# Kernel optimization log

Measured on AMD Instinct MI355X. Metric: run time of the kernel, lower is better.

Reference implementation:

```python
import jax, jax.numpy as jnp
import numpy as np

STEP = 3
INTERVAL = STEP // 2          # 1
W_LEN = 2 * INTERVAL + 1      # sliding window length = 3
N_TOK = 2 * STEP + 1          # tokens per position (reg + window + diff) = 7


def setup_inputs() -> dict:
    key = jax.random.key(0)
    k1, k2, k3, k4 = jax.random.split(key, 4)
    b, n, d, r = 8, 1024, 1024, 256
    x = jax.random.normal(k1, (b, n, d), dtype=jnp.float32)
    mask = jnp.ones((b, N_TOK, 1), dtype=jnp.float32)
    # nn.Linear(input_dim, red_dim, bias=False) weight: (red_dim, input_dim)
    W = jax.random.normal(k2, (r, d), dtype=jnp.float32) / np.sqrt(d).astype(np.float32)
    pos_local = jax.random.normal(k3, (1, N_TOK, r), dtype=jnp.float32)
    reg_token = jax.random.normal(k4, (1, 1, r), dtype=jnp.float32)
    pad_tokens = jnp.zeros((1, INTERVAL, d), dtype=jnp.float32)
    return {"x": x, "mask": mask, "W": W, "pos_local": pos_local,
            "reg_token": reg_token, "pad_tokens": pad_tokens}


def reference(x, mask, W, pos_local, reg_token, pad_tokens):
    # Faithful, vectorized version of the 'local' branch (dropout in eval mode).
    b, n, d = x.shape
    r = W.shape[0]
    pad = jnp.broadcast_to(pad_tokens, (b, INTERVAL, d))
    xp = jnp.concatenate([pad, x, pad], axis=1)            # (b, n + 2*INTERVAL, d)
    # torch loop runs i in [INTERVAL, n): m computed positions; first INTERVAL rows of x_ stay zero
    m = n - INTERVAL
    idx = jnp.arange(m)[:, None] + jnp.arange(W_LEN)[None, :]   # (m, W_LEN), window starts at i-INTERVAL
    wins = xp[:, idx]                                        # (b, m, W_LEN, d)
    center = wins[:, :, INTERVAL][:, :, None, :]             # (b, m, 1, d)
    x_new = jnp.concatenate([wins, wins - center], axis=2)   # (b, m, 2*W_LEN, d)
    y = jnp.einsum('bmwd,rd->bmwr', x_new, W)                # reduce_embedding, no bias
    reg = jnp.broadcast_to(reg_token.reshape(1, 1, 1, r), (b, m, 1, r))
    out = (jnp.concatenate([reg, y], axis=2) + pos_local[None]) * mask[:, None]  # (b, m, N_TOK, r)
    # first INTERVAL sequence positions were never written (remain zero)
    out = jnp.concatenate([jnp.zeros((b, INTERVAL, N_TOK, r), out.dtype), out], axis=1)
    return out
```

## Files before the change

kernel.cpp:

```cpp
#include <hip/hip_runtime.h>

#define BB 8
#define NN 1024
#define DD 1024
#define RR 256
#define MM (BB * NN)
#define NTOK 7

typedef __bf16 bf16x8 __attribute__((ext_vector_type(8)));
typedef float f32x4 __attribute__((ext_vector_type(4)));

__global__ __launch_bounds__(256) void wcvt(const float* __restrict__ W, __bf16* __restrict__ Wb) {
  const int i = (blockIdx.x * 256 + threadIdx.x) * 4;
  float4 v = *reinterpret_cast<const float4*>(W + i);
  union { __bf16 b[4]; ushort4 u; } p;
  p.b[0] = (__bf16)v.x; p.b[1] = (__bf16)v.y; p.b[2] = (__bf16)v.z; p.b[3] = (__bf16)v.w;
  *reinterpret_cast<ushort4*>(Wb + i) = p.u;
}

__device__ __forceinline__ bf16x8 cvt8(const float4& lo, const float4& hi) {
  bf16x8 r;
  r[0] = (__bf16)lo.x; r[1] = (__bf16)lo.y; r[2] = (__bf16)lo.z; r[3] = (__bf16)lo.w;
  r[4] = (__bf16)hi.x; r[5] = (__bf16)hi.y; r[6] = (__bf16)hi.z; r[7] = (__bf16)hi.w;
  return r;
}

__global__ __launch_bounds__(256) void gemm_mfma(const float* __restrict__ X,
                                                 const __bf16* __restrict__ Wb,
                                                 float* __restrict__ P) {
  const int tid = threadIdx.x;
  const int wave = tid >> 6;
  const int lane = tid & 63;
  const int m0 = blockIdx.x * 32;
  const int c0 = wave * 64;
  const int lr = lane & 15;
  const int lg = lane >> 4;

  const float*  xb0 = X  + (size_t)(m0 + lr) * DD + lg * 8;
  const float*  xb1 = xb0 + (size_t)16 * DD;
  const __bf16* wb  = Wb + (size_t)(c0 + lr) * DD + lg * 8;

  f32x4 acc[2][4] = {};

  float4 a0[2][2], a1[2][2];
  bf16x8 b0[4], b1[4];

#define LD_A(dst, kk) do {                                          \
    dst[0][0] = *reinterpret_cast<const float4*>(xb0 + (kk));       \
    dst[0][1] = *reinterpret_cast<const float4*>(xb0 + (kk) + 4);   \
    dst[1][0] = *reinterpret_cast<const float4*>(xb1 + (kk));       \
    dst[1][1] = *reinterpret_cast<const float4*>(xb1 + (kk) + 4);   \
  } while (0)
#define LD_B(dst, kk) do {                                          \
    dst[0] = *reinterpret_cast<const bf16x8*>(wb + (kk));           \
    dst[1] = *reinterpret_cast<const bf16x8*>(wb + 16 * DD + (kk)); \
    dst[2] = *reinterpret_cast<const bf16x8*>(wb + 32 * DD + (kk)); \
    dst[3] = *reinterpret_cast<const bf16x8*>(wb + 48 * DD + (kk)); \
  } while (0)
#define MFMA_STEP(aS, bS) do {                                      \
    bf16x8 af0 = cvt8(aS[0][0], aS[0][1]);                          \
    bf16x8 af1 = cvt8(aS[1][0], aS[1][1]);                          \
    acc[0][0] = __builtin_amdgcn_mfma_f32_16x16x32_bf16(af0, bS[0], acc[0][0], 0, 0, 0); \
    acc[1][0] = __builtin_amdgcn_mfma_f32_16x16x32_bf16(af1, bS[0], acc[1][0], 0, 0, 0); \
    acc[0][1] = __builtin_amdgcn_mfma_f32_16x16x32_bf16(af0, bS[1], acc[0][1], 0, 0, 0); \
    acc[1][1] = __builtin_amdgcn_mfma_f32_16x16x32_bf16(af1, bS[1], acc[1][1], 0, 0, 0); \
    acc[0][2] = __builtin_amdgcn_mfma_f32_16x16x32_bf16(af0, bS[2], acc[0][2], 0, 0, 0); \
    acc[1][2] = __builtin_amdgcn_mfma_f32_16x16x32_bf16(af1, bS[2], acc[1][2], 0, 0, 0); \
    acc[0][3] = __builtin_amdgcn_mfma_f32_16x16x32_bf16(af0, bS[3], acc[0][3], 0, 0, 0); \
    acc[1][3] = __builtin_amdgcn_mfma_f32_16x16x32_bf16(af1, bS[3], acc[1][3], 0, 0, 0); \
  } while (0)

  LD_A(a0, 0); LD_B(b0, 0);
  for (int k0 = 0; k0 < DD - 64; k0 += 64) {
    LD_A(a1, k0 + 32); LD_B(b1, k0 + 32);
    MFMA_STEP(a0, b0);
    LD_A(a0, k0 + 64); LD_B(b0, k0 + 64);
    MFMA_STEP(a1, b1);
  }
  LD_A(a1, DD - 32); LD_B(b1, DD - 32);
  MFMA_STEP(a0, b0);
  MFMA_STEP(a1, b1);

#undef LD_A
#undef LD_B
#undef MFMA_STEP

#pragma unroll
  for (int mi = 0; mi < 2; ++mi)
#pragma unroll
    for (int ni = 0; ni < 4; ++ni) {
      const int col = c0 + ni * 16 + lr;
#pragma unroll
      for (int r = 0; r < 4; ++r) {
        const int row = m0 + mi * 16 + lg * 4 + r;
        P[(size_t)row * RR + col] = acc[mi][ni][r];
      }
    }
}

__global__ void pad_proj(const float* __restrict__ Wt, const float* __restrict__ pad,
                         float* __restrict__ Ppad) {
  const int c = blockIdx.x;
  const int lane = threadIdx.x;
  float s = 0.f;
  for (int k = lane; k < DD; k += 64) s += Wt[(size_t)c * DD + k] * pad[k];
#pragma unroll
  for (int off = 32; off; off >>= 1) s += __shfl_down(s, off);
  if (lane == 0) Ppad[c] = s;
}

__global__ __launch_bounds__(256) void assemble(const float* __restrict__ P,
                                                const float* __restrict__ Ppad,
                                                const float* __restrict__ mask,
                                                const float* __restrict__ pos,
                                                const float* __restrict__ regtok,
                                                float* __restrict__ out) {
  const size_t gid = (size_t)blockIdx.x * blockDim.x + threadIdx.x;
  const int c = (int)(gid & 63) * 4;
  const int j = (int)((gid >> 6) & (NN - 1));
  const int b = (int)(gid >> 16);

  float* outp = out + (((size_t)b * NN + j) * NTOK) * RR + c;

  if (j == 0) {
    float4 z = make_float4(0.f, 0.f, 0.f, 0.f);
#pragma unroll
    for (int t = 0; t < NTOK; ++t)
      *reinterpret_cast<float4*>(outp + (size_t)t * RR) = z;
    return;
  }

  const int i = j - 1;
  float4 q[3];
#pragma unroll
  for (int w = 0; w < 3; ++w) {
    const int src = i + w - 1;
    q[w] = (src < 0)
               ? *reinterpret_cast<const float4*>(Ppad + c)
               : *reinterpret_cast<const float4*>(P + ((size_t)b * NN + src) * RR + c);
  }
  const float4 rg = *reinterpret_cast<const float4*>(regtok + c);

  float mk[NTOK];
#pragma unroll
  for (int t = 0; t < NTOK; ++t) mk[t] = mask[b * NTOK + t];

#pragma unroll
  for (int t = 0; t < NTOK; ++t) {
    const float4 ps = *reinterpret_cast<const float4*>(pos + (size_t)t * RR + c);
    float4 v;
    if (t == 0) {
      v = rg;
    } else if (t <= 3) {
      v = q[t - 1];
    } else {
      const int w = t - 4;
      v = make_float4(q[w].x - q[1].x, q[w].y - q[1].y, q[w].z - q[1].z, q[w].w - q[1].w);
    }
    v.x = (v.x + ps.x) * mk[t];
    v.y = (v.y + ps.y) * mk[t];
    v.z = (v.z + ps.z) * mk[t];
    v.w = (v.w + ps.w) * mk[t];
    *reinterpret_cast<float4*>(outp + (size_t)t * RR) = v;
  }
}

extern "C" void kernel_launch(void* const* d_in, const int* in_sizes, int n_in,
                              void* d_out, int out_size, void* d_ws, size_t ws_size,
                              hipStream_t stream) {
  const float* x      = (const float*)d_in[0];
  const float* mask   = (const float*)d_in[1];
  const float* W      = (const float*)d_in[2];
  const float* pos    = (const float*)d_in[3];
  const float* regtok = (const float*)d_in[4];
  const float* pad    = (const float*)d_in[5];
  float* out = (float*)d_out;

  float*   P    = (float*)d_ws;
  __bf16*  Wb   = (__bf16*)((char*)d_ws + (size_t)MM * RR * 4);
  float*   Ppad = (float*)((char*)d_ws + (size_t)MM * RR * 4 + (size_t)RR * DD * 2);

  wcvt<<<RR * DD / (256 * 4), 256, 0, stream>>>(W, Wb);
  gemm_mfma<<<MM / 32, 256, 0, stream>>>(x, Wb, P);
  pad_proj<<<RR, 64, 0, stream>>>(W, pad, Ppad);
  assemble<<<(BB * NN * 64) / 256, 256, 0, stream>>>(P, Ppad, mask, pos, regtok, out);
}
```

Measured before the change: 138.4 us.

## Fuse output assembly into GEMM epilogue with halo rows and cleanup kernel

The GEMM now produces 16-row tiles, stages them in shared memory, and directly writes the 7-token output for the interior positions of each tile, so the full projection matrix no longer has to round-trip through global memory. Only the two boundary rows at each tile edge go to a halo buffer, and a small cleanup kernel fills in the output positions whose windows cross tile edges. Halving the M tile cuts per-block reuse of the W operand, which doubles W reads, and adds LDS use and an extra launch.

```diff
diff --git a/kernel.cpp b/kernel.cpp
--- a/kernel.cpp
+++ b/kernel.cpp
@@ -18,6 +18,17 @@
   *reinterpret_cast<ushort4*>(Wb + i) = p.u;
 }
 
+__global__ void pad_proj(const float* __restrict__ Wt, const float* __restrict__ pad,
+                         float* __restrict__ Ppad) {
+  const int c = blockIdx.x;
+  const int lane = threadIdx.x;
+  float s = 0.f;
+  for (int k = lane; k < DD; k += 64) s += Wt[(size_t)c * DD + k] * pad[k];
+#pragma unroll
+  for (int off = 32; off; off >>= 1) s += __shfl_down(s, off);
+  if (lane == 0) Ppad[c] = s;
+}
+
 __device__ __forceinline__ bf16x8 cvt8(const float4& lo, const float4& hi) {
   bf16x8 r;
   r[0] = (__bf16)lo.x; r[1] = (__bf16)lo.y; r[2] = (__bf16)lo.z; r[3] = (__bf16)lo.w;
@@ -25,31 +36,32 @@
   return r;
 }
 
-__global__ __launch_bounds__(256) void gemm_mfma(const float* __restrict__ X,
-                                                 const __bf16* __restrict__ Wb,
-                                                 float* __restrict__ P) {
+__global__ __launch_bounds__(256) void gemm_fused(const float* __restrict__ X,
+                                                  const __bf16* __restrict__ Wb,
+                                                  const float* __restrict__ Ppad,
+                                                  const float* __restrict__ mask,
+                                                  const float* __restrict__ pos,
+                                                  const float* __restrict__ regtok,
+                                                  float* __restrict__ Phalo,
+                                                  float* __restrict__ out) {
   const int tid = threadIdx.x;
   const int wave = tid >> 6;
   const int lane = tid & 63;
-  const int m0 = blockIdx.x * 32;
+  const int m0 = blockIdx.x * 16;
   const int c0 = wave * 64;
   const int lr = lane & 15;
   const int lg = lane >> 4;
 
-  const float*  xb0 = X  + (size_t)(m0 + lr) * DD + lg * 8;
-  const float*  xb1 = xb0 + (size_t)16 * DD;
-  const __bf16* wb  = Wb + (size_t)(c0 + lr) * DD + lg * 8;
-
-  f32x4 acc[2][4] = {};
-
-  float4 a0[2][2], a1[2][2];
-  bf16x8 b0[4], b1[4];
+  const float*  xb = X  + (size_t)(m0 + lr) * DD + lg * 8;
+  const __bf16* wb = Wb + (size_t)(c0 + lr) * DD + lg * 8;
+
+  f32x4 acc[4] = {};
+  float4 aA[2], aB[2];
+  bf16x8 bA[4], bB[4];
 
 #define LD_A(dst, kk) do {                                          \
-    dst[0][0] = *reinterpret_cast<const float4*>(xb0 + (kk));       \
-    dst[0][1] = *reinterpret_cast<const float4*>(xb0 + (kk) + 4);   \
-    dst[1][0] = *reinterpret_cast<const float4*>(xb1 + (kk));       \
-    dst[1][1] = *reinterpret_cast<const float4*>(xb1 + (kk) + 4);   \
+    dst[0] = *reinterpret_cast<const float4*>(xb + (kk));           \
+    dst[1] = *reinterpret_cast<const float4*>(xb + (kk) + 4);       \
   } while (0)
 #define LD_B(dst, kk) do {                                          \
     dst[0] = *reinterpret_cast<const bf16x8*>(wb + (kk));           \
@@ -58,96 +70,120 @@
     dst[3] = *reinterpret_cast<const bf16x8*>(wb + 48 * DD + (kk)); \
   } while (0)
 #define MFMA_STEP(aS, bS) do {                                      \
-    bf16x8 af0 = cvt8(aS[0][0], aS[0][1]);                          \
-    bf16x8 af1 = cvt8(aS[1][0], aS[1][1]);                          \
-    acc[0][0] = __builtin_amdgcn_mfma_f32_16x16x32_bf16(af0, bS[0], acc[0][0], 0, 0, 0); \
-    acc[1][0] = __builtin_amdgcn_mfma_f32_16x16x32_bf16(af1, bS[0], acc[1][0], 0, 0, 0); \
-    acc[0][1] = __builtin_amdgcn_mfma_f32_16x16x32_bf16(af0, bS[1], acc[0][1], 0, 0, 0); \
-    acc[1][1] = __builtin_amdgcn_mfma_f32_16x16x32_bf16(af1, bS[1], acc[1][1], 0, 0, 0); \
-    acc[0][2] = __builtin_amdgcn_mfma_f32_16x16x32_bf16(af0, bS[2], acc[0][2], 0, 0, 0); \
-    acc[1][2] = __builtin_amdgcn_mfma_f32_16x16x32_bf16(af1, bS[2], acc[1][2], 0, 0, 0); \
-    acc[0][3] = __builtin_amdgcn_mfma_f32_16x16x32_bf16(af0, bS[3], acc[0][3], 0, 0, 0); \
-    acc[1][3] = __builtin_amdgcn_mfma_f32_16x16x32_bf16(af1, bS[3], acc[1][3], 0, 0, 0); \
+    bf16x8 af = cvt8(aS[0], aS[1]);                                 \
+    acc[0] = __builtin_amdgcn_mfma_f32_16x16x32_bf16(af, bS[0], acc[0], 0, 0, 0); \
+    acc[1] = __builtin_amdgcn_mfma_f32_16x16x32_bf16(af, bS[1], acc[1], 0, 0, 0); \
+    acc[2] = __builtin_amdgcn_mfma_f32_16x16x32_bf16(af, bS[2], acc[2], 0, 0, 0); \
+    acc[3] = __builtin_amdgcn_mfma_f32_16x16x32_bf16(af, bS[3], acc[3], 0, 0, 0); \
   } while (0)
 
-  LD_A(a0, 0); LD_B(b0, 0);
+  LD_A(aA, 0); LD_B(bA, 0);
   for (int k0 = 0; k0 < DD - 64; k0 += 64) {
-    LD_A(a1, k0 + 32); LD_B(b1, k0 + 32);
-    MFMA_STEP(a0, b0);
-    LD_A(a0, k0 + 64); LD_B(b0, k0 + 64);
-    MFMA_STEP(a1, b1);
-  }
-  LD_A(a1, DD - 32); LD_B(b1, DD - 32);
-  MFMA_STEP(a0, b0);
-  MFMA_STEP(a1, b1);
+    LD_A(aB, k0 + 32); LD_B(bB, k0 + 32);
+    MFMA_STEP(aA, bA);
+    LD_A(aA, k0 + 64); LD_B(bA, k0 + 64);
+    MFMA_STEP(aB, bB);
+  }
+  LD_A(aB, DD - 32); LD_B(bB, DD - 32);
+  MFMA_STEP(aA, bA);
+  MFMA_STEP(aB, bB);
 
 #undef LD_A
 #undef LD_B
 #undef MFMA_STEP
 
-#pragma unroll
-  for (int mi = 0; mi < 2; ++mi)
-#pragma unroll
-    for (int ni = 0; ni < 4; ++ni) {
-      const int col = c0 + ni * 16 + lr;
-#pragma unroll
-      for (int r = 0; r < 4; ++r) {
-        const int row = m0 + mi * 16 + lg * 4 + r;
-        P[(size_t)row * RR + col] = acc[mi][ni][r];
+  __shared__ float Pt[16][260];
+#pragma unroll
+  for (int ni = 0; ni < 4; ++ni)
+#pragma unroll
+    for (int r = 0; r < 4; ++r)
+      Pt[lg * 4 + r][c0 + ni * 16 + lr] = acc[ni][r];
+  __syncthreads();
+
+  const int c4 = (tid & 63) * 4;
+
+  {
+    const int hr = tid >> 6;
+    const int row = (hr < 2) ? hr : hr + 12;
+    float4 v = *reinterpret_cast<const float4*>(&Pt[row][c4]);
+    *reinterpret_cast<float4*>(&Phalo[(size_t)(m0 + row) * RR + c4]) = v;
+  }
+
+  const int b  = m0 >> 10;
+  const int n0 = m0 & (NN - 1);
+
+  float mk[NTOK];
+#pragma unroll
+  for (int t = 0; t < NTOK; ++t) mk[t] = mask[b * NTOK + t];
+  const float4 rg = *reinterpret_cast<const float4*>(regtok + c4);
+  float4 psv[NTOK];
+#pragma unroll
+  for (int t = 0; t < NTOK; ++t)
+    psv[t] = *reinterpret_cast<const float4*>(pos + (size_t)t * RR + c4);
+
+  const int jlo = (n0 == 0) ? 0 : n0 + 2;
+  for (int j = jlo + wave; j < n0 + 16; j += 4) {
+    float* outp = out + (((size_t)b * NN + j) * NTOK) * RR + c4;
+    if (j == 0) {
+      float4 z = make_float4(0.f, 0.f, 0.f, 0.f);
+#pragma unroll
+      for (int t = 0; t < NTOK; ++t)
+        *reinterpret_cast<float4*>(outp + (size_t)t * RR) = z;
+      continue;
+    }
+    float4 q[3];
+#pragma unroll
+    for (int w = 0; w < 3; ++w) {
+      const int src = j - 2 + w;
+      q[w] = (src < 0) ? *reinterpret_cast<const float4*>(Ppad + c4)
+                       : *reinterpret_cast<const float4*>(&Pt[src - n0][c4]);
+    }
+#pragma unroll
+    for (int t = 0; t < NTOK; ++t) {
+      float4 v;
+      if (t == 0) {
+        v = rg;
+      } else if (t <= 3) {
+        v = q[t - 1];
+      } else {
+        const int w = t - 4;
+        v = make_float4(q[w].x - q[1].x, q[w].y - q[1].y, q[w].z - q[1].z, q[w].w - q[1].w);
       }
-    }
-}
-
-__global__ void pad_proj(const float* __restrict__ Wt, const float* __restrict__ pad,
-                         float* __restrict__ Ppad) {
-  const int c = blockIdx.x;
-  const int lane = threadIdx.x;
-  float s = 0.f;
-  for (int k = lane; k < DD; k += 64) s += Wt[(size_t)c * DD + k] * pad[k];
-#pragma unroll
-  for (int off = 32; off; off >>= 1) s += __shfl_down(s, off);
-  if (lane == 0) Ppad[c] = s;
-}
-
-__global__ __launch_bounds__(256) void assemble(const float* __restrict__ P,
-                                                const float* __restrict__ Ppad,
-                                                const float* __restrict__ mask,
-                                                const float* __restrict__ pos,
-                                                const float* __restrict__ regtok,
-                                                float* __restrict__ out) {
-  const size_t gid = (size_t)blockIdx.x * blockDim.x + threadIdx.x;
-  const int c = (int)(gid & 63) * 4;
-  const int j = (int)((gid >> 6) & (NN - 1));
-  const int b = (int)(gid >> 16);
-
-  float* outp = out + (((size_t)b * NN + j) * NTOK) * RR + c;
-
-  if (j == 0) {
-    float4 z = make_float4(0.f, 0.f, 0.f, 0.f);
-#pragma unroll
-    for (int t = 0; t < NTOK; ++t)
-      *reinterpret_cast<float4*>(outp + (size_t)t * RR) = z;
-    return;
-  }
-
-  const int i = j - 1;
+      v.x = (v.x + psv[t].x) * mk[t];
+      v.y = (v.y + psv[t].y) * mk[t];
+      v.z = (v.z + psv[t].z) * mk[t];
+      v.w = (v.w + psv[t].w) * mk[t];
+      *reinterpret_cast<float4*>(outp + (size_t)t * RR) = v;
+    }
+  }
+}
+
+#define NCLEAN_ROWS (BB * 126)
+__global__ __launch_bounds__(256) void cleanup(const float* __restrict__ Phalo,
+                                               const float* __restrict__ mask,
+                                               const float* __restrict__ pos,
+                                               const float* __restrict__ regtok,
+                                               float* __restrict__ out) {
+  const int gid = blockIdx.x * 256 + threadIdx.x;
+  const int rowIdx = gid >> 6;
+  if (rowIdx >= NCLEAN_ROWS) return;
+  const int b  = rowIdx / 126;
+  const int rr = rowIdx - b * 126;
+  const int j  = 16 * ((rr >> 1) + 1) + (rr & 1);
+  const int c4 = (gid & 63) * 4;
+
   float4 q[3];
 #pragma unroll
-  for (int w = 0; w < 3; ++w) {
-    const int src = i + w - 1;
-    q[w] = (src < 0)
-               ? *reinterpret_cast<const float4*>(Ppad + c)
-               : *reinterpret_cast<const float4*>(P + ((size_t)b * NN + src) * RR + c);
-  }
-  const float4 rg = *reinterpret_cast<const float4*>(regtok + c);
-
-  float mk[NTOK];
-#pragma unroll
-  for (int t = 0; t < NTOK; ++t) mk[t] = mask[b * NTOK + t];
+  for (int w = 0; w < 3; ++w)
+    q[w] = *reinterpret_cast<const float4*>(&Phalo[((size_t)b * NN + j - 2 + w) * RR + c4]);
+
+  const float4 rg = *reinterpret_cast<const float4*>(regtok + c4);
+  float* outp = out + (((size_t)b * NN + j) * NTOK) * RR + c4;
 
 #pragma unroll
   for (int t = 0; t < NTOK; ++t) {
-    const float4 ps = *reinterpret_cast<const float4*>(pos + (size_t)t * RR + c);
+    const float4 ps = *reinterpret_cast<const float4*>(pos + (size_t)t * RR + c4);
+    const float m = mask[b * NTOK + t];
     float4 v;
     if (t == 0) {
       v = rg;
@@ -157,10 +193,10 @@
       const int w = t - 4;
       v = make_float4(q[w].x - q[1].x, q[w].y - q[1].y, q[w].z - q[1].z, q[w].w - q[1].w);
     }
-    v.x = (v.x + ps.x) * mk[t];
-    v.y = (v.y + ps.y) * mk[t];
-    v.z = (v.z + ps.z) * mk[t];
-    v.w = (v.w + ps.w) * mk[t];
+    v.x = (v.x + ps.x) * m;
+    v.y = (v.y + ps.y) * m;
+    v.z = (v.z + ps.z) * m;
+    v.w = (v.w + ps.w) * m;
     *reinterpret_cast<float4*>(outp + (size_t)t * RR) = v;
   }
 }
@@ -176,12 +212,12 @@
   const float* pad    = (const float*)d_in[5];
   float* out = (float*)d_out;
 
-  float*   P    = (float*)d_ws;
-  __bf16*  Wb   = (__bf16*)((char*)d_ws + (size_t)MM * RR * 4);
-  float*   Ppad = (float*)((char*)d_ws + (size_t)MM * RR * 4 + (size_t)RR * DD * 2);
+  float*  Phalo = (float*)d_ws;
+  __bf16* Wb    = (__bf16*)((char*)d_ws + (size_t)MM * RR * 4);
+  float*  Ppad  = (float*)((char*)d_ws + (size_t)MM * RR * 4 + (size_t)RR * DD * 2);
 
   wcvt<<<RR * DD / (256 * 4), 256, 0, stream>>>(W, Wb);
-  gemm_mfma<<<MM / 32, 256, 0, stream>>>(x, Wb, P);
   pad_proj<<<RR, 64, 0, stream>>>(W, pad, Ppad);
-  assemble<<<(BB * NN * 64) / 256, 256, 0, stream>>>(P, Ppad, mask, pos, regtok, out);
-}
+  gemm_fused<<<MM / 16, 256, 0, stream>>>(x, Wb, Ppad, mask, pos, regtok, Phalo, out);
+  cleanup<<<NCLEAN_ROWS * 64 / 256, 256, 0, stream>>>(Phalo, mask, pos, regtok, out);
+}
```

Measured after the change: 148.0 us. 1.07x slower.
